# Kernel tuning notes

Hardware: AMD Instinct MI355X
Metric: run time of the kernel (lower is better)

The kernel has to match this reference:

```python
import jax, jax.numpy as jnp
import numpy as np

D_MODEL = 1024
N_HEADS = 16
D_FF = 4096
WINDOW = 256
EPS = 1e-5


def setup_inputs() -> dict:
    key = jax.random.key(0)
    ks = jax.random.split(key, 12)
    B, T, C = 4, 1024, D_MODEL
    s = lambda fan: 1.0 / np.sqrt(fan)
    return {
        "x": jax.random.normal(ks[0], (B, T, C), jnp.float32),
        "Wqkv": jax.random.normal(ks[1], (3 * C, C), jnp.float32) * s(C),
        "bqkv": jnp.zeros((3 * C,), jnp.float32),
        "Wo": jax.random.normal(ks[2], (C, C), jnp.float32) * s(C),
        "bo": jnp.zeros((C,), jnp.float32),
        "W1": jax.random.normal(ks[3], (D_FF, C), jnp.float32) * s(C),
        "b1": jnp.zeros((D_FF,), jnp.float32),
        "W2": jax.random.normal(ks[4], (C, D_FF), jnp.float32) * s(D_FF),
        "b2": jnp.zeros((C,), jnp.float32),
        "g1": jnp.ones((C,), jnp.float32),
        "be1": jnp.zeros((C,), jnp.float32),
        "g2": jnp.ones((C,), jnp.float32),
        "be2": jnp.zeros((C,), jnp.float32),
    }


def _layernorm(x, g, b):
    mu = jnp.mean(x, axis=-1, keepdims=True)
    var = jnp.mean(jnp.square(x - mu), axis=-1, keepdims=True)
    return (x - mu) * jax.lax.rsqrt(var + EPS) * g + b


def reference(x, Wqkv, bqkv, Wo, bo, W1, b1, W2, b2, g1, be1, g2, be2):
    B, T, C = x.shape
    H, Dh = N_HEADS, C // N_HEADS
    # QKV projection (torch MultiheadAttention packed in_proj)
    qkv = jnp.einsum("btc,ec->bte", x, Wqkv) + bqkv  # [B,T,3C]
    q, k, v = jnp.split(qkv, 3, axis=-1)
    q = q.reshape(B, T, H, Dh).transpose(0, 2, 1, 3)  # [B,H,T,Dh]
    k = k.reshape(B, T, H, Dh).transpose(0, 2, 1, 3)
    v = v.reshape(B, T, H, Dh).transpose(0, 2, 1, 3)
    scores = jnp.einsum("bhqd,bhkd->bhqk", q, k) / jnp.sqrt(jnp.float32(Dh))
    # causal banded mask: key j visible to query i iff 0 <= i-j < WINDOW
    i = jnp.arange(T)[:, None]
    j = jnp.arange(T)[None, :]
    band = (j <= i) & (i - j < WINDOW)
    scores = jnp.where(band, scores, -jnp.inf)
    attn = jax.nn.softmax(scores, axis=-1)
    ctx = jnp.einsum("bhqk,bhkd->bhqd", attn, v)  # [B,H,T,Dh]
    ctx = ctx.transpose(0, 2, 1, 3).reshape(B, T, C)
    attn_out = jnp.einsum("btc,oc->bto", ctx, Wo) + bo
    x = _layernorm(x + attn_out, g1, be1)
    h = jax.nn.gelu(jnp.einsum("btc,fc->btf", x, W1) + b1, approximate=False)
    ffn_out = jnp.einsum("btf,cf->btc", h, W2) + b2
    return _layernorm(x + ffn_out, g2, be2)
```

## Files before the change

### kernel.cpp

```cpp
#include <hip/hip_runtime.h>
#include <hip/hip_bf16.h>

typedef __attribute__((ext_vector_type(4))) float floatx4;
typedef __attribute__((ext_vector_type(8))) short shortx8;

struct bf4 { __hip_bfloat16 h[4]; };
union U8 { shortx8 v; __hip_bfloat16 h[8]; };
union U4 { unsigned long long v; __hip_bfloat16 h[4]; };

__device__ __forceinline__ void async_copy16(const __hip_bfloat16* g, __hip_bfloat16* l) {
  __builtin_amdgcn_global_load_lds((__attribute__((address_space(1))) void*)g,
                                   (__attribute__((address_space(3))) void*)l,
                                   16, 0, 0);
}

__global__ __launch_bounds__(256) void cast_all_kernel(
    const float* __restrict__ s0, __hip_bfloat16* __restrict__ d0, int nb0,
    const float* __restrict__ s1, __hip_bfloat16* __restrict__ d1, int nb1,
    const float* __restrict__ s2, __hip_bfloat16* __restrict__ d2, int nb2,
    const float* __restrict__ s3, __hip_bfloat16* __restrict__ d3, int nb3,
    const float* __restrict__ s4, __hip_bfloat16* __restrict__ d4) {
  int b = blockIdx.x;
  const float* src; __hip_bfloat16* dst;
  if (b < nb0) { src = s0; dst = d0; }
  else { b -= nb0;
    if (b < nb1) { src = s1; dst = d1; }
    else { b -= nb1;
      if (b < nb2) { src = s2; dst = d2; }
      else { b -= nb2;
        if (b < nb3) { src = s3; dst = d3; }
        else { b -= nb3; src = s4; dst = d4; }
      }
    }
  }
  const int i = b * 256 + threadIdx.x;
  const float4 v = ((const float4*)src)[i];
  bf4 o4;
  o4.h[0] = __float2bfloat16(v.x);
  o4.h[1] = __float2bfloat16(v.y);
  o4.h[2] = __float2bfloat16(v.z);
  o4.h[3] = __float2bfloat16(v.w);
  *(bf4*)(dst + (size_t)i * 4) = o4;
}

#define STG_A(slot, kt, ks)                                                    \
  async_copy16(Ag + (size_t)(kt) * 64 + (size_t)(ks) * 32,                     \
               &As[slot][tid * 8]);                                            \
  async_copy16(Ag + (size_t)128 * K + (size_t)(kt) * 64 + (size_t)(ks) * 32,   \
               &As[slot][4096 + tid * 8]);

#define STG_B(slot, kt, ks)                                                    \
  async_copy16(Bg + (size_t)(kt) * 64 + (size_t)(ks) * 32,                     \
               &Bs[slot][tid * 8]);                                            \
  async_copy16(Bg + (size_t)128 * K + (size_t)(kt) * 64 + (size_t)(ks) * 32,   \
               &Bs[slot][4096 + tid * 8]);

#define G256_READ_A(dst, slot, mh)                                             \
  _Pragma("unroll")                                                            \
  for (int i_ = 0; i_ < 4; ++i_)                                               \
    dst[i_] = *(const shortx8*)&As[slot][ard + ((mh) * 4 + i_) * 512];

#define G256_READ_B(dst, slot)                                                 \
  _Pragma("unroll")                                                            \
  for (int i_ = 0; i_ < 4; ++i_)                                               \
    dst[i_] = *(const shortx8*)&Bs[slot][brd + i_ * 512];

#define G256_MFMA(afr, bfr, MH)                                                \
  __builtin_amdgcn_sched_barrier(0);                                           \
  __builtin_amdgcn_s_setprio(1);                                               \
  _Pragma("unroll")                                                            \
  for (int mi_ = 0; mi_ < 4; ++mi_)                                            \
    _Pragma("unroll")                                                          \
    for (int ni_ = 0; ni_ < 4; ++ni_)                                          \
      acc[(MH) * 4 + mi_][ni_] = __builtin_amdgcn_mfma_f32_16x16x32_bf16(      \
          afr[mi_], bfr[ni_], acc[(MH) * 4 + mi_][ni_], 0, 0, 0);              \
  __builtin_amdgcn_s_setprio(0);                                               \
  __builtin_amdgcn_sched_barrier(0);

#define G256_BAR() asm volatile("s_barrier" ::: "memory")

#define G256_KLOOP()                                                           \
  STG_A(0, 0, 0) STG_B(0, 0, 0)                                                \
  STG_A(1, 0, 1) STG_B(1, 0, 1)                                                \
  STG_A(2, 1, 0) STG_B(2, 1, 0)                                                \
  asm volatile("s_waitcnt vmcnt(8)" ::: "memory");                             \
  G256_BAR();                                                                  \
  shortx8 a0[4], a1[4], bE[4], bO[4];                                          \
  G256_READ_B(bE, 0)                                                           \
  G256_READ_A(a0, 0, 0)                                                        \
  for (int T = 0; T < NKT; ++T) {                                              \
    const int s00 = (2 * T) & 3;                                               \
    const int s01 = (2 * T + 1) & 3;                                           \
    const int sx  = (2 * T + 2) & 3;                           \
    const int sn1 = (2 * T + 3) & 3;                           \
    const int sn0 = (2 * T + 4) & 3;                           \
    const bool st1 = (T + 1 < NKT);                                            \
    const bool st2 = (T + 2 < NKT);                                            \
                                                                       \
    G256_BAR();                                                                \
    if (st1) { asm volatile("s_waitcnt vmcnt(4)" ::: "memory"); }              \
    else     { asm volatile("s_waitcnt vmcnt(0)" ::: "memory"); }              \
    G256_READ_A(a1, s00, 1)                                                    \
    if (st1) { STG_A(sn1, T + 1, 1) }                                          \
    G256_MFMA(a0, bE, 0)                                                       \
                                                                       \
    G256_BAR();                                                                \
    G256_READ_B(bO, s01)                                                       \
    G256_READ_A(a0, s01, 0)                                                    \
    if (st1) { STG_B(sn1, T + 1, 1) }                                          \
    G256_MFMA(a1, bE, 1)                                                       \
                                                                       \
    G256_BAR();                                                                \
    if (st1) { asm volatile("s_waitcnt vmcnt(4)" ::: "memory"); }              \
    else     { asm volatile("s_waitcnt vmcnt(0)" ::: "memory"); }              \
    G256_READ_A(a1, s01, 1)                                                    \
    if (st2) { STG_A(sn0, T + 2, 0) }                                          \
    G256_MFMA(a0, bO, 0)                                                       \
                                                                       \
    G256_BAR();                                                                \
    if (st1) {                                                                 \
      G256_READ_B(bE, sx)                                                      \
      G256_READ_A(a0, sx, 0)                                                   \
    }                                                                          \
    if (st2) { STG_B(sn0, T + 2, 0) }                                          \
    G256_MFMA(a1, bO, 1)                                                       \
  }

template<int EPI>
__global__ __launch_bounds__(512, 2) void gemm256(
    const __hip_bfloat16* __restrict__ A,
    const __hip_bfloat16* __restrict__ B,
    const float* __restrict__ bias,
    __hip_bfloat16* __restrict__ outb,
    int M, int N, int K, int NT)
{
  __shared__ __align__(16) __hip_bfloat16 As[4][256 * 32];
  __shared__ __align__(16) __hip_bfloat16 Bs[4][256 * 32];
  const int tid  = threadIdx.x;
  const int lane = tid & 63;
  const int wave = tid >> 6;
  const int wr = wave >> 2;
  const int wc = wave & 3;
  const int fr = lane & 15;
  const int fq = lane >> 4;

  const int nwg = gridDim.x;
  const int cpx = nwg >> 3;
  const int swz = (blockIdx.x & 7) * cpx + (blockIdx.x >> 3);
  const int mt = swz / NT, nt = swz % NT;
  const long bm = (long)mt * 256, bn = (long)nt * 256;

  const int srow = tid >> 2;
  const int sch  = (tid & 3) ^ ((tid >> 3) & 3);
  const __hip_bfloat16* Ag = A + (bm + srow) * (size_t)K + sch * 8;
  const __hip_bfloat16* Bg = B + (bn + srow) * (size_t)K + sch * 8;

  const int swc = (fq ^ ((fr >> 1) & 3)) << 3;
  const int ard = (wr * 128 + fr) * 32 + swc;
  const int brd = (wc * 64 + fr) * 32 + swc;

  const floatx4 zero = {0.f, 0.f, 0.f, 0.f};
  floatx4 acc[8][4];
#pragma unroll
  for (int mi = 0; mi < 8; ++mi)
#pragma unroll
    for (int ni = 0; ni < 4; ++ni) acc[mi][ni] = zero;

  const int NKT = K >> 6;
  G256_KLOOP()

#pragma unroll
  for (int mi = 0; mi < 8; ++mi) {
#pragma unroll
    for (int ni = 0; ni < 4; ++ni) {
      const long col = bn + wc * 64 + ni * 16 + fr;
      const float bv = bias[col];
#pragma unroll
      for (int r = 0; r < 4; ++r) {
        const long row = bm + wr * 128 + mi * 16 + fq * 4 + r;
        float v = acc[mi][ni][r] + bv;
        if (EPI == 1) {
          const float u = v + 0.044715f * v * v * v;
          v = v / (1.0f + __expf(-1.5957691216057308f * u));
        }
        outb[(size_t)row * N + col] = __float2bfloat16(v);
      }
    }
  }
}

__global__ __launch_bounds__(512, 2) void gemm256_splitk(
    const __hip_bfloat16* __restrict__ A,
    const __hip_bfloat16* __restrict__ B,
    __hip_bfloat16* __restrict__ part,
    int M, int N, int K, int Klen, int NT, int TPS)
{
  __shared__ __align__(16) __hip_bfloat16 As[4][256 * 32];
  __shared__ __align__(16) __hip_bfloat16 Bs[4][256 * 32];
  const int tid  = threadIdx.x;
  const int lane = tid & 63;
  const int wave = tid >> 6;
  const int wr = wave >> 2;
  const int wc = wave & 3;
  const int fr = lane & 15;
  const int fq = lane >> 4;

  const int nwg = gridDim.x;
  const int cpx = nwg >> 3;
  const int swz = (blockIdx.x & 7) * cpx + (blockIdx.x >> 3);
  const int zt = swz / TPS;
  const int tile = swz % TPS;
  const int mt = tile / NT, nt = tile % NT;
  const long bm = (long)mt * 256, bn = (long)nt * 256;
  const int kstart = zt * Klen;

  const int srow = tid >> 2;
  const int sch  = (tid & 3) ^ ((tid >> 3) & 3);
  const __hip_bfloat16* Ag = A + (bm + srow) * (size_t)K + kstart + sch * 8;
  const __hip_bfloat16* Bg = B + (bn + srow) * (size_t)K + kstart + sch * 8;

  const int swc = (fq ^ ((fr >> 1) & 3)) << 3;
  const int ard = (wr * 128 + fr) * 32 + swc;
  const int brd = (wc * 64 + fr) * 32 + swc;

  const floatx4 zero = {0.f, 0.f, 0.f, 0.f};
  floatx4 acc[8][4];
#pragma unroll
  for (int mi = 0; mi < 8; ++mi)
#pragma unroll
    for (int ni = 0; ni < 4; ++ni) acc[mi][ni] = zero;

  const int NKT = Klen >> 6;
  G256_KLOOP()

  __hip_bfloat16* outp = part + (size_t)zt * M * N;
#pragma unroll
  for (int mi = 0; mi < 8; ++mi) {
#pragma unroll
    for (int ni = 0; ni < 4; ++ni) {
      const long col = bn + wc * 64 + ni * 16 + fr;
#pragma unroll
      for (int r = 0; r < 4; ++r) {
        const long row = bm + wr * 128 + mi * 16 + fq * 4 + r;
        outp[(size_t)row * N + col] = __float2bfloat16(acc[mi][ni][r]);
      }
    }
  }
}

#define GEMM_SWIZZLE()                                                        \
  const int flat = blockIdx.x + gridDim.x * (blockIdx.y + 32 * blockIdx.z);   \
  const int xcd_ = flat & 7;                                                  \
  int rsw_ = flat >> 3;                                                       \
  const int mt_ = xcd_ * 4 + (rsw_ & 3);                                      \
  rsw_ >>= 2;                                                                 \
  const int nt_ = rsw_ % gridDim.x;                                           \
  const int zt_ = rsw_ / gridDim.x;

#define GEMM_STAGE(buf, koff)                                      \
  async_copy16(Ag0 + (koff),           &Asl[buf][tid * 8]);        \
  async_copy16(Ag0 + (koff) + rstride, &Asl[buf][tid * 8 + 2048]); \
  async_copy16(Bg0 + (koff),           &Bsl[buf][tid * 8]);        \
  async_copy16(Bg0 + (koff) + rstride, &Bsl[buf][tid * 8 + 2048]);

#define GEMM_KLOOP(NI)                                                        \
  GEMM_STAGE(0, 0)                                                            \
  GEMM_STAGE(1, 32)                                                           \
  int cur = 0;                                                                \
  for (int it = 0; it < (NI); ++it) {                                         \
    if (it + 2 < (NI)) {                                                      \
      const int nb = (cur >= 1) ? cur - 1 : cur + 2;           \
      GEMM_STAGE(nb, (it + 2) * 32)                                           \
      asm volatile("s_waitcnt vmcnt(8)" ::: "memory");                        \
    } else if (it + 1 < (NI)) {                                               \
      asm volatile("s_waitcnt vmcnt(4)" ::: "memory");                        \
    } else {                                                                  \
      asm volatile("s_waitcnt vmcnt(0)" ::: "memory");                        \
    }                                                                         \
    asm volatile("s_barrier" ::: "memory");                                   \
    const __hip_bfloat16* Ac = Asl[cur];                                      \
    const __hip_bfloat16* Bc = Bsl[cur];                                      \
    shortx8 afr[4], bfr[4];                                                   \
    _Pragma("unroll")                                                         \
    for (int i = 0; i < 4; ++i) {                                             \
      afr[i] = *(const shortx8*)&Ac[(wr * 64 + i * 16 + fr) * 32 + sw];       \
      bfr[i] = *(const shortx8*)&Bc[(wc * 64 + i * 16 + fr) * 32 + sw];       \
    }                                                                         \
    _Pragma("unroll")                                                         \
    for (int mi = 0; mi < 4; ++mi)                                            \
      _Pragma("unroll")                                                       \
      for (int ni = 0; ni < 4; ++ni)                                          \
        acc[mi][ni] = __builtin_amdgcn_mfma_f32_16x16x32_bf16(                \
            afr[mi], bfr[ni], acc[mi][ni], 0, 0, 0);                          \
    asm volatile("s_barrier" ::: "memory");                                   \
    cur = (cur == 2) ? 0 : cur + 1;                                           \
  }

__global__ __launch_bounds__(256) void gemm_bt_splitk(
    const __hip_bfloat16* __restrict__ A,
    const __hip_bfloat16* __restrict__ B,
    __hip_bfloat16* __restrict__ part,
    int M, int N, int K, int Klen)
{
  __shared__ __align__(16) __hip_bfloat16 Asl[3][128 * 32];
  __shared__ __align__(16) __hip_bfloat16 Bsl[3][128 * 32];
  const int tid  = threadIdx.x;
  const int lane = tid & 63;
  const int wave = tid >> 6;
  const int wr = wave >> 1, wc = wave & 1;
  GEMM_SWIZZLE()
  const long bm = (long)mt_ * 128, bn = (long)nt_ * 128;
  const int kstart = zt_ * Klen;

  const int srow = tid >> 2;
  const int scol = ((((tid & 3) - (tid >> 3)) & 3) << 3);
  const __hip_bfloat16* Ag0 = A + (bm + srow) * (long)K + kstart + scol;
  const __hip_bfloat16* Bg0 = B + (bn + srow) * (long)K + kstart + scol;
  const long rstride = 64l * K;

  const int fr = lane & 15;
  const int fq = lane >> 4;
  const int sw = (((fq + ((fr >> 1) & 3)) & 3) << 3);

  const floatx4 zero = {0.f, 0.f, 0.f, 0.f};
  floatx4 acc[4][4];
#pragma unroll
  for (int mi = 0; mi < 4; ++mi)
#pragma unroll
    for (int ni = 0; ni < 4; ++ni) acc[mi][ni] = zero;

  const int NI = Klen >> 5;
  GEMM_KLOOP(NI)

  __hip_bfloat16* outp = part + (size_t)zt_ * M * N;
#pragma unroll
  for (int mi = 0; mi < 4; ++mi) {
#pragma unroll
    for (int ni = 0; ni < 4; ++ni) {
      const long col = bn + wc * 64 + ni * 16 + fr;
#pragma unroll
      for (int r = 0; r < 4; ++r) {
        const long row = bm + wr * 64 + mi * 16 + fq * 4 + r;
        outp[(size_t)row * N + col] = __float2bfloat16(acc[mi][ni][r]);
      }
    }
  }
}

__global__ __launch_bounds__(256) void transpose_v_kernel(
    const __hip_bfloat16* __restrict__ qkv, __hip_bfloat16* __restrict__ vt)
{
  const int bh = blockIdx.y;
  const int tt = blockIdx.x;
  const int b = bh >> 4, h = bh & 15;
  __shared__ __hip_bfloat16 tile[64][65];
  const int tid = threadIdx.x;
  const int r = tid >> 2;
  const int c = (tid & 3) << 4;
  const __hip_bfloat16* src = qkv + (size_t)(b * 1024 + tt * 64 + r) * 3072 + 2048 + h * 64 + c;
  U8 u0, u1;
  u0.v = *(const shortx8*)src;
  u1.v = *(const shortx8*)(src + 8);
#pragma unroll
  for (int j = 0; j < 8; ++j) { tile[r][c + j] = u0.h[j]; tile[r][c + 8 + j] = u1.h[j]; }
  __syncthreads();
  U8 w0, w1;
#pragma unroll
  for (int j = 0; j < 8; ++j) { w0.h[j] = tile[c + j][r]; w1.h[j] = tile[c + 8 + j][r]; }
  __hip_bfloat16* dst = vt + ((size_t)bh * 64 + r) * 1024 + tt * 64 + c;
  *(shortx8*)dst       = w0.v;
  *(shortx8*)(dst + 8) = w1.v;
}

__global__ __launch_bounds__(256) void attn_kernel(
    const __hip_bfloat16* __restrict__ qkv,
    const __hip_bfloat16* __restrict__ vt,
    __hip_bfloat16* __restrict__ ctx)
{
  const int wave = threadIdx.x >> 6;
  const int lane = threadIdx.x & 63;
  const int gw = blockIdx.x * 4 + wave;
  const int qt = gw & 63;
  const int bh = gw >> 6;
  const int b = bh >> 4, h = bh & 15;
  const int fr = lane & 15, fq = lane >> 4;
  const int q0 = qt << 4;

  __shared__ __align__(16) __hip_bfloat16 Plds[4][16 * 32];
  __hip_bfloat16* Pw = Plds[wave];

  const __hip_bfloat16* qrow = qkv + (size_t)(b * 1024 + q0 + fr) * 3072 + h * 64;
  const shortx8 aq0 = *(const shortx8*)(qrow + fq * 8);
  const shortx8 aq1 = *(const shortx8*)(qrow + 32 + fq * 8);

  const float SC = 0.125f * 1.44269504088896f;
  float m_r[4] = {-1e30f, -1e30f, -1e30f, -1e30f};
  float l_r[4] = {0.f, 0.f, 0.f, 0.f};
  const floatx4 zero = {0.f, 0.f, 0.f, 0.f};
  floatx4 o[4];
#pragma unroll
  for (int nd = 0; nd < 4; ++nd) o[nd] = zero;

  const int kt0 = (q0 >= 255) ? ((q0 - 255) >> 5) : 0;
  const int kt1 = (q0 + 15) >> 5;
  for (int kt = kt0; kt <= kt1; ++kt) {
    const int kbase = kt << 5;
    const __hip_bfloat16* krow0 = qkv + (size_t)(b * 1024 + kbase + fr) * 3072 + 1024 + h * 64;
    const __hip_bfloat16* krow1 = krow0 + 16 * 3072;
    const shortx8 bk00 = *(const shortx8*)(krow0 + fq * 8);
    const shortx8 bk01 = *(const shortx8*)(krow0 + 32 + fq * 8);
    const shortx8 bk10 = *(const shortx8*)(krow1 + fq * 8);
    const shortx8 bk11 = *(const shortx8*)(krow1 + 32 + fq * 8);
    floatx4 s0 = zero, s1 = zero;
    s0 = __builtin_amdgcn_mfma_f32_16x16x32_bf16(aq0, bk00, s0, 0, 0, 0);
    s0 = __builtin_amdgcn_mfma_f32_16x16x32_bf16(aq1, bk01, s0, 0, 0, 0);
    s1 = __builtin_amdgcn_mfma_f32_16x16x32_bf16(aq0, bk10, s1, 0, 0, 0);
    s1 = __builtin_amdgcn_mfma_f32_16x16x32_bf16(aq1, bk11, s1, 0, 0, 0);
#pragma unroll
    for (int r = 0; r < 4; ++r) { s0[r] *= SC; s1[r] *= SC; }
    if (kbase + 31 > q0 || kbase < q0 - 240) {
#pragma unroll
      for (int r = 0; r < 4; ++r) {
        const int tq = q0 + fq * 4 + r;
        const int j0 = kbase + fr;
        const int j1 = j0 + 16;
        if (j0 > tq || j0 < tq - 255) s0[r] = -3e38f;
        if (j1 > tq || j1 < tq - 255) s1[r] = -3e38f;
      }
    }
#pragma unroll
    for (int r = 0; r < 4; ++r) {
      float vmax = fmaxf(s0[r], s1[r]);
      vmax = fmaxf(vmax, __shfl_xor(vmax, 1));
      vmax = fmaxf(vmax, __shfl_xor(vmax, 2));
      vmax = fmaxf(vmax, __shfl_xor(vmax, 4));
      vmax = fmaxf(vmax, __shfl_xor(vmax, 8));
      const float mnew = fmaxf(m_r[r], vmax);
      const float alpha = exp2f(m_r[r] - mnew);
      const float p0 = exp2f(s0[r] - mnew);
      const float p1 = exp2f(s1[r] - mnew);
      m_r[r] = mnew;
      float ps = p0 + p1;
      ps += __shfl_xor(ps, 1);
      ps += __shfl_xor(ps, 2);
      ps += __shfl_xor(ps, 4);
      ps += __shfl_xor(ps, 8);
      l_r[r] = l_r[r] * alpha + ps;
      o[0][r] *= alpha; o[1][r] *= alpha; o[2][r] *= alpha; o[3][r] *= alpha;
      Pw[(fq * 4 + r) * 32 + fr]      = __float2bfloat16(p0);
      Pw[(fq * 4 + r) * 32 + 16 + fr] = __float2bfloat16(p1);
    }
    asm volatile("s_waitcnt lgkmcnt(0)" ::: "memory");
    const shortx8 ap = *(const shortx8*)&Pw[fr * 32 + fq * 8];
#pragma unroll
    for (int nd = 0; nd < 4; ++nd) {
      const shortx8 bv = *(const shortx8*)&vt[((size_t)bh * 64 + nd * 16 + fr) * 1024 + kbase + fq * 8];
      o[nd] = __builtin_amdgcn_mfma_f32_16x16x32_bf16(ap, bv, o[nd], 0, 0, 0);
    }
    asm volatile("s_waitcnt lgkmcnt(0)" ::: "memory");
  }
#pragma unroll
  for (int nd = 0; nd < 4; ++nd)
#pragma unroll
    for (int r = 0; r < 4; ++r)
      ctx[(size_t)(b * 1024 + q0 + fq * 4 + r) * 1024 + h * 64 + nd * 16 + fr] =
          __float2bfloat16(o[nd][r] / l_r[r]);
}

template<int S, int WB>
__global__ __launch_bounds__(256) void ln_sum_kernel(
    const __hip_bfloat16* __restrict__ part,
    const float* __restrict__ resid,
    const float* __restrict__ bias,
    const float* __restrict__ g, const float* __restrict__ be,
    float* __restrict__ outf, __hip_bfloat16* __restrict__ outb)
{
  const int row = blockIdx.x;
  const int tid = threadIdx.x;
  const size_t base = (size_t)row * 1024;
  float4 v = ((const float4*)(resid + base))[tid];
  const float4 bv = ((const float4*)bias)[tid];
  v.x += bv.x; v.y += bv.y; v.z += bv.z; v.w += bv.w;
#pragma unroll
  for (int s = 0; s < S; ++s) {
    U4 p;
    p.v = *(const unsigned long long*)&part[(size_t)s * 4096 * 1024 + base + tid * 4];
    v.x += __bfloat162float(p.h[0]);
    v.y += __bfloat162float(p.h[1]);
    v.z += __bfloat162float(p.h[2]);
    v.w += __bfloat162float(p.h[3]);
  }
  float sm = v.x + v.y + v.z + v.w;
  float ss = v.x * v.x + v.y * v.y + v.z * v.z + v.w * v.w;
#pragma unroll
  for (int off = 1; off < 64; off <<= 1) {
    sm += __shfl_xor(sm, off);
    ss += __shfl_xor(ss, off);
  }
  __shared__ float red[8];
  if ((tid & 63) == 0) { red[tid >> 6] = sm; red[4 + (tid >> 6)] = ss; }
  __syncthreads();
  sm = red[0] + red[1] + red[2] + red[3];
  ss = red[4] + red[5] + red[6] + red[7];
  const float mu = sm * (1.0f / 1024.0f);
  const float rs = rsqrtf(ss * (1.0f / 1024.0f) - mu * mu + 1e-5f);
  const float4 gg = ((const float4*)g)[tid];
  const float4 bb = ((const float4*)be)[tid];
  float4 y;
  y.x = (v.x - mu) * rs * gg.x + bb.x;
  y.y = (v.y - mu) * rs * gg.y + bb.y;
  y.z = (v.z - mu) * rs * gg.z + bb.z;
  y.w = (v.w - mu) * rs * gg.w + bb.w;
  ((float4*)(outf + base))[tid] = y;
  if (WB) {
    bf4 o4;
    o4.h[0] = __float2bfloat16(y.x);
    o4.h[1] = __float2bfloat16(y.y);
    o4.h[2] = __float2bfloat16(y.z);
    o4.h[3] = __float2bfloat16(y.w);
    *(bf4*)(outb + base + tid * 4) = o4;
  }
}

extern "C" void kernel_launch(void* const* d_in, const int* in_sizes, int n_in,
                              void* d_out, int out_size, void* d_ws, size_t ws_size,
                              hipStream_t stream) {
  const float* x    = (const float*)d_in[0];
  const float* Wqkv = (const float*)d_in[1];
  const float* bqkv = (const float*)d_in[2];
  const float* Wo   = (const float*)d_in[3];
  const float* bo   = (const float*)d_in[4];
  const float* W1   = (const float*)d_in[5];
  const float* b1   = (const float*)d_in[6];
  const float* W2   = (const float*)d_in[7];
  const float* b2   = (const float*)d_in[8];
  const float* g1   = (const float*)d_in[9];
  const float* be1  = (const float*)d_in[10];
  const float* g2   = (const float*)d_in[11];
  const float* be2  = (const float*)d_in[12];

  char* ws = (char*)d_ws;
  size_t off = 0;
  auto alloc = [&](size_t bytes) -> void* {
    void* p = ws + off;
    off += (bytes + 255) & ~(size_t)255;
    return p;
  };
  __hip_bfloat16* wqkvb = (__hip_bfloat16*)alloc(6291456);
  __hip_bfloat16* wob   = (__hip_bfloat16*)alloc(2097152);
  __hip_bfloat16* w1b   = (__hip_bfloat16*)alloc(8388608);
  __hip_bfloat16* w2b   = (__hip_bfloat16*)alloc(8388608);
  __hip_bfloat16* xb    = (__hip_bfloat16*)alloc(8388608);
  __hip_bfloat16* qkvb  = (__hip_bfloat16*)alloc(25165824);
  __hip_bfloat16* vtb   = (__hip_bfloat16*)alloc(8388608);
  __hip_bfloat16* ctxb  = (__hip_bfloat16*)alloc(8388608);
  __hip_bfloat16* part  = (__hip_bfloat16*)alloc(4u * 8388608);
  float*          x1f   = (float*)alloc(16777216);
  __hip_bfloat16* x1b   = (__hip_bfloat16*)alloc(8388608);
  __hip_bfloat16* hb    = (__hip_bfloat16*)alloc(33554432);
  (void)ws_size; (void)in_sizes; (void)n_in; (void)out_size;

  cast_all_kernel<<<16384, 256, 0, stream>>>(x, xb, 4096,
                                             Wqkv, wqkvb, 3072,
                                             Wo, wob, 1024,
                                             W1, w1b, 4096,
                                             W2, w2b);
  gemm256<0><<<192, 512, 0, stream>>>(xb, wqkvb, bqkv, qkvb, 4096, 3072, 1024, 12);
  transpose_v_kernel<<<dim3(16, 64), 256, 0, stream>>>(qkvb, vtb);
  attn_kernel<<<1024, 256, 0, stream>>>(qkvb, vtb, ctxb);
  gemm_bt_splitk<<<dim3(8, 32, 2), 256, 0, stream>>>(ctxb, wob, part, 4096, 1024, 1024, 512);
  ln_sum_kernel<2, 1><<<4096, 256, 0, stream>>>(part, x, bo, g1, be1, x1f, x1b);
  gemm256<1><<<256, 512, 0, stream>>>(x1b, w1b, b1, hb, 4096, 4096, 1024, 16);
  gemm256_splitk<<<256, 512, 0, stream>>>(hb, w2b, part, 4096, 1024, 4096, 1024, 4, 64);
  ln_sum_kernel<4, 0><<<4096, 256, 0, stream>>>(part, x1f, b2, g2, be2, (float*)d_out, nullptr);
}
```

Measured before the change: 321.2 us.

## Restructure GEMM k-loop into uniform four-slot ring with full-tile MFMA steps

Replaces the irregular half-tile A/B staging schedule with a uniform pipeline. Each 32-wide k-chunk is staged as one A+B unit into a four-slot LDS ring, with one full 8x4 MFMA block per chunk, double-buffered register fragments, and explicit vmcnt/lgkmcnt waits. Global pointers are now incremented in place rather than recomputed from offsets. This aims to simplify the wait and barrier pattern and keep loads further ahead of compute. In exchange it holds more fragment registers per wave, which risks register pressure, and it assumes an even number of 64-wide k tiles.

```diff
diff --git a/kernel.cpp b/kernel.cpp
--- a/kernel.cpp
+++ b/kernel.cpp
@@ -43,88 +43,68 @@
   *(bf4*)(dst + (size_t)i * 4) = o4;
 }
 
-#define STG_A(slot, kt, ks)                                                    \
-  async_copy16(Ag + (size_t)(kt) * 64 + (size_t)(ks) * 32,                     \
-               &As[slot][tid * 8]);                                            \
-  async_copy16(Ag + (size_t)128 * K + (size_t)(kt) * 64 + (size_t)(ks) * 32,   \
-               &As[slot][4096 + tid * 8]);
-
-#define STG_B(slot, kt, ks)                                                    \
-  async_copy16(Bg + (size_t)(kt) * 64 + (size_t)(ks) * 32,                     \
-               &Bs[slot][tid * 8]);                                            \
-  async_copy16(Bg + (size_t)128 * K + (size_t)(kt) * 64 + (size_t)(ks) * 32,   \
-               &Bs[slot][4096 + tid * 8]);
-
-#define G256_READ_A(dst, slot, mh)                                             \
+#define G3_STAGE(k)                                                            \
+  async_copy16(AgLo + (k) * 32, &As[(k) & 3][tid * 8]);                        \
+  async_copy16(AgHi + (k) * 32, &As[(k) & 3][4096 + tid * 8]);                 \
+  async_copy16(BgLo + (k) * 32, &Bs[(k) & 3][tid * 8]);                        \
+  async_copy16(BgHi + (k) * 32, &Bs[(k) & 3][4096 + tid * 8]);
+
+#define G3_READS(fa, fb, slot)                                                 \
   _Pragma("unroll")                                                            \
-  for (int i_ = 0; i_ < 4; ++i_)                                               \
-    dst[i_] = *(const shortx8*)&As[slot][ard + ((mh) * 4 + i_) * 512];
-
-#define G256_READ_B(dst, slot)                                                 \
+  for (int m_ = 0; m_ < 8; ++m_)                                               \
+    fa[m_] = *(const shortx8*)&As[slot][ard + m_ * 512];                       \
   _Pragma("unroll")                                                            \
-  for (int i_ = 0; i_ < 4; ++i_)                                               \
-    dst[i_] = *(const shortx8*)&Bs[slot][brd + i_ * 512];
-
-#define G256_MFMA(afr, bfr, MH)                                                \
+  for (int n_ = 0; n_ < 4; ++n_)                                               \
+    fb[n_] = *(const shortx8*)&Bs[slot][brd + n_ * 512];
+
+#define G3_MFMA(fa, fb)                                                        \
   __builtin_amdgcn_sched_barrier(0);                                           \
   __builtin_amdgcn_s_setprio(1);                                               \
   _Pragma("unroll")                                                            \
-  for (int mi_ = 0; mi_ < 4; ++mi_)                                            \
+  for (int m_ = 0; m_ < 8; ++m_)                                               \
     _Pragma("unroll")                                                          \
-    for (int ni_ = 0; ni_ < 4; ++ni_)                                          \
-      acc[(MH) * 4 + mi_][ni_] = __builtin_amdgcn_mfma_f32_16x16x32_bf16(      \
-          afr[mi_], bfr[ni_], acc[(MH) * 4 + mi_][ni_], 0, 0, 0);              \
+    for (int n_ = 0; n_ < 4; ++n_)                                             \
+      acc[m_][n_] = __builtin_amdgcn_mfma_f32_16x16x32_bf16(                   \
+          fa[m_], fb[n_], acc[m_][n_], 0, 0, 0);                               \
   __builtin_amdgcn_s_setprio(0);                                               \
   __builtin_amdgcn_sched_barrier(0);
 
-#define G256_BAR() asm volatile("s_barrier" ::: "memory")
-
-#define G256_KLOOP()                                                           \
-  STG_A(0, 0, 0) STG_B(0, 0, 0)                                                \
-  STG_A(1, 0, 1) STG_B(1, 0, 1)                                                \
-  STG_A(2, 1, 0) STG_B(2, 1, 0)                                                \
-  asm volatile("s_waitcnt vmcnt(8)" ::: "memory");                             \
-  G256_BAR();                                                                  \
-  shortx8 a0[4], a1[4], bE[4], bO[4];                                          \
-  G256_READ_B(bE, 0)                                                           \
-  G256_READ_A(a0, 0, 0)                                                        \
-  for (int T = 0; T < NKT; ++T) {                                              \
-    const int s00 = (2 * T) & 3;                                               \
-    const int s01 = (2 * T + 1) & 3;                                           \
-    const int sx  = (2 * T + 2) & 3;                           \
-    const int sn1 = (2 * T + 3) & 3;                           \
-    const int sn0 = (2 * T + 4) & 3;                           \
-    const bool st1 = (T + 1 < NKT);                                            \
-    const bool st2 = (T + 2 < NKT);                                            \
-                                                                       \
-    G256_BAR();                                                                \
-    if (st1) { asm volatile("s_waitcnt vmcnt(4)" ::: "memory"); }              \
-    else     { asm volatile("s_waitcnt vmcnt(0)" ::: "memory"); }              \
-    G256_READ_A(a1, s00, 1)                                                    \
-    if (st1) { STG_A(sn1, T + 1, 1) }                                          \
-    G256_MFMA(a0, bE, 0)                                                       \
-                                                                       \
-    G256_BAR();                                                                \
-    G256_READ_B(bO, s01)                                                       \
-    G256_READ_A(a0, s01, 0)                                                    \
-    if (st1) { STG_B(sn1, T + 1, 1) }                                          \
-    G256_MFMA(a1, bE, 1)                                                       \
-                                                                       \
-    G256_BAR();                                                                \
-    if (st1) { asm volatile("s_waitcnt vmcnt(4)" ::: "memory"); }              \
-    else     { asm volatile("s_waitcnt vmcnt(0)" ::: "memory"); }              \
-    G256_READ_A(a1, s01, 1)                                                    \
-    if (st2) { STG_A(sn0, T + 2, 0) }                                          \
-    G256_MFMA(a0, bO, 0)                                                       \
-                                                                       \
-    G256_BAR();                                                                \
-    if (st1) {                                                                 \
-      G256_READ_B(bE, sx)                                                      \
-      G256_READ_A(a0, sx, 0)                                                   \
-    }                                                                          \
-    if (st2) { STG_B(sn0, T + 2, 0) }                                          \
-    G256_MFMA(a1, bO, 1)                                                       \
-  }
+#define G3_BAR()   asm volatile("s_barrier" ::: "memory")
+#define G3_LGKM0() asm volatile("s_waitcnt lgkmcnt(0)" ::: "memory")
+#define G3_VM(n)   asm volatile("s_waitcnt vmcnt(" #n ")" ::: "memory")
+
+#define G3_KLOOP()                                                             \
+  shortx8 fa0[8], fb0[4], fa1[8], fb1[4];                                      \
+  G3_STAGE(0) G3_STAGE(1) G3_STAGE(2) G3_STAGE(3)                              \
+  G3_VM(8); G3_BAR();                                                          \
+  G3_READS(fa0, fb0, 0)                                                        \
+  G3_LGKM0();                                                                  \
+  const int NIT = (NKT - 2) >> 1;                                              \
+  for (int it = 0; it < NIT; ++it) {                                           \
+    G3_VM(8); G3_BAR();                                                        \
+    G3_READS(fa1, fb1, 1) G3_STAGE(4)                                          \
+    G3_MFMA(fa0, fb0) G3_LGKM0();                                              \
+    G3_VM(8); G3_BAR();                                                        \
+    G3_READS(fa0, fb0, 2) G3_STAGE(5)                                          \
+    G3_MFMA(fa1, fb1) G3_LGKM0();                                              \
+    G3_VM(8); G3_BAR();                                                        \
+    G3_READS(fa1, fb1, 3) G3_STAGE(6)                                          \
+    G3_MFMA(fa0, fb0) G3_LGKM0();                                              \
+    G3_VM(8); G3_BAR();                                                        \
+    G3_READS(fa0, fb0, 0) G3_STAGE(7)                                          \
+    G3_MFMA(fa1, fb1) G3_LGKM0();                                              \
+    AgLo += 128; AgHi += 128; BgLo += 128; BgHi += 128;                        \
+  }                                                                            \
+  G3_VM(8); G3_BAR();                                                          \
+  G3_READS(fa1, fb1, 1)                                                        \
+  G3_MFMA(fa0, fb0) G3_LGKM0();                                                \
+  G3_VM(4); G3_BAR();                                                          \
+  G3_READS(fa0, fb0, 2)                                                        \
+  G3_MFMA(fa1, fb1) G3_LGKM0();                                                \
+  G3_VM(0); G3_BAR();                                                          \
+  G3_READS(fa1, fb1, 3)                                                        \
+  G3_MFMA(fa0, fb0) G3_LGKM0();                                                \
+  G3_MFMA(fa1, fb1)
 
 template<int EPI>
 __global__ __launch_bounds__(512, 2) void gemm256(
@@ -152,8 +132,10 @@
 
   const int srow = tid >> 2;
   const int sch  = (tid & 3) ^ ((tid >> 3) & 3);
-  const __hip_bfloat16* Ag = A + (bm + srow) * (size_t)K + sch * 8;
-  const __hip_bfloat16* Bg = B + (bn + srow) * (size_t)K + sch * 8;
+  const __hip_bfloat16* AgLo = A + (bm + srow) * (size_t)K + sch * 8;
+  const __hip_bfloat16* AgHi = AgLo + (size_t)128 * K;
+  const __hip_bfloat16* BgLo = B + (bn + srow) * (size_t)K + sch * 8;
+  const __hip_bfloat16* BgHi = BgLo + (size_t)128 * K;
 
   const int swc = (fq ^ ((fr >> 1) & 3)) << 3;
   const int ard = (wr * 128 + fr) * 32 + swc;
@@ -167,7 +149,7 @@
     for (int ni = 0; ni < 4; ++ni) acc[mi][ni] = zero;
 
   const int NKT = K >> 6;
-  G256_KLOOP()
+  G3_KLOOP()
 
 #pragma unroll
   for (int mi = 0; mi < 8; ++mi) {
@@ -216,8 +198,10 @@
 
   const int srow = tid >> 2;
   const int sch  = (tid & 3) ^ ((tid >> 3) & 3);
-  const __hip_bfloat16* Ag = A + (bm + srow) * (size_t)K + kstart + sch * 8;
-  const __hip_bfloat16* Bg = B + (bn + srow) * (size_t)K + kstart + sch * 8;
+  const __hip_bfloat16* AgLo = A + (bm + srow) * (size_t)K + kstart + sch * 8;
+  const __hip_bfloat16* AgHi = AgLo + (size_t)128 * K;
+  const __hip_bfloat16* BgLo = B + (bn + srow) * (size_t)K + kstart + sch * 8;
+  const __hip_bfloat16* BgHi = BgLo + (size_t)128 * K;
 
   const int swc = (fq ^ ((fr >> 1) & 3)) << 3;
   const int ard = (wr * 128 + fr) * 32 + swc;
@@ -231,7 +215,7 @@
     for (int ni = 0; ni < 4; ++ni) acc[mi][ni] = zero;
 
   const int NKT = Klen >> 6;
-  G256_KLOOP()
+  G3_KLOOP()
 
   __hip_bfloat16* outp = part + (size_t)zt * M * N;
 #pragma unroll
```

Result: slower. 329.1 us (+2.5%).
